# Kernel optimization log

Measured on AMD Instinct MI355X. Metric: run time of the kernel, lower is better.

Reference implementation:

```python
import jax, jax.numpy as jnp
import numpy as np

B, T, D = 64, 256, 1024
H, HS = 16, 64
FF = 4096
EPS = 1e-5


def _layernorm(x, g, b):
    mu = jnp.mean(x, axis=-1, keepdims=True)
    var = jnp.mean(jnp.square(x - mu), axis=-1, keepdims=True)
    return (x - mu) * jax.lax.rsqrt(var + EPS) * g + b


def setup_inputs() -> dict:
    key = jax.random.key(0)
    ks = jax.random.split(key, 12)
    s = 0.02
    return {
        "x": jax.random.normal(ks[0], (B, T, D), jnp.float32),
        "ln1_g": jnp.ones((D,), jnp.float32),
        "ln1_b": jnp.zeros((D,), jnp.float32),
        "Wq": jax.random.normal(ks[1], (H, D, HS), jnp.float32) * s,
        "Wk": jax.random.normal(ks[2], (H, D, HS), jnp.float32) * s,
        "Wv": jax.random.normal(ks[3], (H, D, HS), jnp.float32) * s,
        "Wproj": jax.random.normal(ks[4], (D, D), jnp.float32) * s,
        "bproj": jnp.zeros((D,), jnp.float32),
        "ln2_g": jnp.ones((D,), jnp.float32),
        "ln2_b": jnp.zeros((D,), jnp.float32),
        "W1": jax.random.normal(ks[5], (D, FF), jnp.float32) * s,
        "b1": jnp.zeros((FF,), jnp.float32),
        "W2": jax.random.normal(ks[6], (FF, D), jnp.float32) * s,
        "b2": jnp.zeros((D,), jnp.float32),
    }


def reference(x, ln1_g, ln1_b, Wq, Wk, Wv, Wproj, bproj, ln2_g, ln2_b, W1, b1, W2, b2):
    # x = ln1(x)
    h = _layernorm(x, ln1_g, ln1_b)
    # per-head Q/K/V projections, batched over heads
    q = jnp.einsum("btd,hde->bhte", h, Wq)
    k = jnp.einsum("btd,hde->bhte", h, Wk)
    v = jnp.einsum("btd,hde->bhte", h, Wv)
    # NOTE: source scales by C**-0.5 with C = input_size (D), not head_size
    scale = D ** -0.5
    scores = jnp.einsum("bhte,bhse->bhts", q, k) * scale
    causal = jnp.tril(jnp.ones((T, T), bool))
    scores = jnp.where(causal, scores, -jnp.inf)
    w = jax.nn.softmax(scores, axis=-1)  # dropout is identity in eval
    attn = jnp.einsum("bhts,bhse->bthe", w, v).reshape(x.shape[0], x.shape[1], H * HS)
    sa = attn @ Wproj + bproj
    # residual onto ln1 output (as written in source)
    y = h + sa
    h2 = _layernorm(y, ln2_g, ln2_b)
    ff = jax.nn.relu(h2 @ W1 + b1) @ W2 + b2
    return h2 + ff
```

## Files before the change

kernel.cpp:

```cpp
#include <hip/hip_runtime.h>

typedef __bf16 bf16x8 __attribute__((ext_vector_type(8)));
typedef float f32x4 __attribute__((ext_vector_type(4)));
typedef unsigned short ushort_t;

__device__ __forceinline__ ushort_t f2bf(float f) {
  unsigned int u = __float_as_uint(f);
  u += 0x7fffu + ((u >> 16) & 1u);
  return (ushort_t)(u >> 16);
}
__device__ __forceinline__ float bf2f(ushort_t u) {
  return __uint_as_float(((unsigned int)u) << 16);
}

__device__ __forceinline__ void gl_lds16(const ushort_t* g, const char* l) {
  __builtin_amdgcn_global_load_lds(
      (const __attribute__((address_space(1))) void*)g,
      (__attribute__((address_space(3))) void*)l, 16, 0, 0);
}

__global__ __launch_bounds__(256) void fill_k(float* __restrict__ p, long n, float v) {
  long i = (long)blockIdx.x * 256 + threadIdx.x;
  if (i < n) p[i] = v;
}

__global__ __launch_bounds__(256) void transpose_w(const float* __restrict__ in,
                                                   ushort_t* __restrict__ out,
                                                   int R, int C) {
  __shared__ float tile[32][33];
  const float* inb = in + (long)blockIdx.z * R * C;
  ushort_t* outb = out + (long)blockIdx.z * R * C;
  int r0 = blockIdx.x * 32, c0 = blockIdx.y * 32;
  int tx = threadIdx.x & 31, ty = threadIdx.x >> 5;
#pragma unroll
  for (int i = ty; i < 32; i += 8) tile[i][tx] = inb[(long)(r0 + i) * C + (c0 + tx)];
  __syncthreads();
#pragma unroll
  for (int i = ty; i < 32; i += 8) outb[(long)(c0 + i) * R + (r0 + tx)] = f2bf(tile[tx][i]);
}

template <bool BFIN>
__global__ __launch_bounds__(256) void ln_k(const void* __restrict__ xin,
                                            const float* __restrict__ g,
                                            const float* __restrict__ b,
                                            ushort_t* __restrict__ outU) {
  __shared__ float red[8];
  long row = blockIdx.x;
  int tid = threadIdx.x;
  float4 v;
  if constexpr (BFIN) {
    ushort4 u4 = ((const ushort4*)((const ushort_t*)xin + row * 1024))[tid];
    v = make_float4(bf2f(u4.x), bf2f(u4.y), bf2f(u4.z), bf2f(u4.w));
  } else {
    v = ((const float4*)((const float*)xin + row * 1024))[tid];
  }
  float s = v.x + v.y + v.z + v.w;
#pragma unroll
  for (int off = 32; off; off >>= 1) s += __shfl_xor(s, off);
  int w = tid >> 6;
  if ((tid & 63) == 0) red[w] = s;
  __syncthreads();
  float mean = (red[0] + red[1] + red[2] + red[3]) * (1.0f / 1024.0f);
  float dx = v.x - mean, dy = v.y - mean, dz = v.z - mean, dw = v.w - mean;
  float s2 = dx * dx + dy * dy + dz * dz + dw * dw;
#pragma unroll
  for (int off = 32; off; off >>= 1) s2 += __shfl_xor(s2, off);
  if ((tid & 63) == 0) red[4 + w] = s2;
  __syncthreads();
  float var = (red[4] + red[5] + red[6] + red[7]) * (1.0f / 1024.0f);
  float rstd = rsqrtf(var + 1e-5f);
  int c = tid * 4;
  ushort4 u;
  u.x = f2bf(dx * rstd * g[c + 0] + b[c + 0]);
  u.y = f2bf(dy * rstd * g[c + 1] + b[c + 1]);
  u.z = f2bf(dz * rstd * g[c + 2] + b[c + 2]);
  u.w = f2bf(dw * rstd * g[c + 3] + b[c + 3]);
  ((ushort4*)(outU + row * 1024))[tid] = u;
}

template <int EPI>
__global__ __launch_bounds__(512, 2) void gemm256(const ushort_t* __restrict__ A,
                                                  const ushort_t* __restrict__ Bt,
                                                  int M, int N, int K, int NBC,
                                                  const float* __restrict__ bias,
                                                  const ushort_t* __restrict__ resU,
                                                  float* __restrict__ outF,
                                                  ushort_t* __restrict__ outU,
                                                  ushort_t* __restrict__ outU2,
                                                  ushort_t* __restrict__ outU3) {
  __shared__ __align__(16) char lds[131072];
  const int tid = threadIdx.x;
  const int lane = tid & 63;
  const int w = tid >> 6;
  const int wr = w >> 2, wc = w & 3;
  const int g = lane >> 4, lr = lane & 15;
  const int cpx = gridDim.x >> 3;
  const int wg = (blockIdx.x & 7) * cpx + (blockIdx.x >> 3);
  const long m0 = (long)(wg / NBC) * 256;
  const long n0 = (long)(wg % NBC) * 256;
  const int srow = tid >> 3;
  const int sslot = (tid & 7) ^ (srow & 7);
  const ushort_t* sA = A + (m0 + srow) * (long)K + sslot * 8;
  const ushort_t* sB = Bt + (n0 + srow) * (long)K + sslot * 8;
  const int dA = tid * 16;
  const int dB = 32768 + tid * 16;
  const int abase = (wr * 128 + lr) * 128;
  const int bbase = 32768 + (wc * 64 + lr) * 128;
  const int s0 = g ^ (lr & 7);
  const int s1 = (4 + g) ^ (lr & 7);
  const int NT = K >> 6;

  f32x4 acc[8][4] = {};
  bf16x8 aR[4][2], bR[4][2];
  const char* rb;

#define STAGE_A(tile, half) do {                                          \
    const long _ko = (long)(tile) * 64;                                   \
    char* _d = lds + (((tile) & 1) << 16) + ((half) << 14) + dA;          \
    gl_lds16(sA + _ko + (long)(2 * (half)) * 64 * K, _d);                 \
    gl_lds16(sA + _ko + (long)(2 * (half) + 1) * 64 * K, _d + 8192);      \
  } while (0)
#define STAGE_B(tile, half) do {                                          \
    const long _ko = (long)(tile) * 64;                                   \
    char* _d = lds + (((tile) & 1) << 16) + ((half) << 14) + dB;          \
    gl_lds16(sB + _ko + (long)(2 * (half)) * 64 * K, _d);                 \
    gl_lds16(sB + _ko + (long)(2 * (half) + 1) * 64 * K, _d + 8192);      \
  } while (0)
#define RD_A(base_mf) do {                                                \
    _Pragma("unroll") for (int mf = 0; mf < 4; ++mf) {                    \
      aR[mf][0] = *(const bf16x8*)(rb + abase + ((base_mf) + mf) * 2048 + s0 * 16); \
      aR[mf][1] = *(const bf16x8*)(rb + abase + ((base_mf) + mf) * 2048 + s1 * 16); \
    } } while (0)
#define RD_B2(base_nf) do {                                               \
    _Pragma("unroll") for (int nf = 0; nf < 2; ++nf) {                    \
      bR[(base_nf) + nf][0] = *(const bf16x8*)(rb + bbase + ((base_nf) + nf) * 2048 + s0 * 16); \
      bR[(base_nf) + nf][1] = *(const bf16x8*)(rb + bbase + ((base_nf) + nf) * 2048 + s1 * 16); \
    } } while (0)
#define QUAD(MB, NB) do {                                                 \
    __builtin_amdgcn_s_setprio(1);                                        \
    _Pragma("unroll") for (int mf = 0; mf < 4; ++mf)                      \
      _Pragma("unroll") for (int nf = 0; nf < 2; ++nf) {                  \
        acc[(MB) + mf][(NB) + nf] = __builtin_amdgcn_mfma_f32_16x16x32_bf16(aR[mf][0], bR[(NB) + nf][0], acc[(MB) + mf][(NB) + nf], 0, 0, 0); \
        acc[(MB) + mf][(NB) + nf] = __builtin_amdgcn_mfma_f32_16x16x32_bf16(aR[mf][1], bR[(NB) + nf][1], acc[(MB) + mf][(NB) + nf], 0, 0, 0); \
      }                                                                   \
    __builtin_amdgcn_s_setprio(0); } while (0)
#define LGKM0 do {                                                        \
    asm volatile("s_waitcnt lgkmcnt(0)" ::: "memory");                    \
    __builtin_amdgcn_sched_barrier(0); } while (0)

  STAGE_B(0, 0); STAGE_B(0, 1); STAGE_A(0, 0); STAGE_A(0, 1);
  STAGE_B(1, 0); STAGE_B(1, 1); STAGE_A(1, 0);
  asm volatile("s_waitcnt vmcnt(6)" ::: "memory");
  __builtin_amdgcn_s_barrier();

  for (int t = 0; t < NT; t += 2) {
    const bool s2 = (t + 2 < NT), s3 = (t + 3 < NT);
    rb = lds;
    RD_A(0);
    RD_B2(0);
    STAGE_A(t + 1, 1);
    asm volatile("s_waitcnt lgkmcnt(8)" ::: "memory");
    __builtin_amdgcn_s_barrier();
    LGKM0;
    QUAD(0, 0);
    __builtin_amdgcn_s_barrier();
    RD_B2(2);
    __builtin_amdgcn_s_barrier();
    LGKM0;
    QUAD(0, 2);
    __builtin_amdgcn_s_barrier();
    if (s2) STAGE_B(t + 2, 0);
    RD_A(4);
    __builtin_amdgcn_s_barrier();
    LGKM0;
    QUAD(4, 2);
    __builtin_amdgcn_s_barrier();
    if (s2) { STAGE_B(t + 2, 1); STAGE_A(t + 2, 0); }
    __builtin_amdgcn_s_barrier();
    QUAD(4, 0);
    if (s2) asm volatile("s_waitcnt vmcnt(6)" ::: "memory");
    else    asm volatile("s_waitcnt vmcnt(0)" ::: "memory");
    __builtin_amdgcn_s_barrier();
    rb = lds + 65536;
    RD_A(0);
    RD_B2(0);
    if (s2) STAGE_A(t + 2, 1);
    asm volatile("s_waitcnt lgkmcnt(8)" ::: "memory");
    __builtin_amdgcn_s_barrier();
    LGKM0;
    QUAD(0, 0);
    __builtin_amdgcn_s_barrier();
    RD_B2(2);
    __builtin_amdgcn_s_barrier();
    LGKM0;
    QUAD(0, 2);
    __builtin_amdgcn_s_barrier();
    if (s3) STAGE_B(t + 3, 0);
    RD_A(4);
    __builtin_amdgcn_s_barrier();
    LGKM0;
    QUAD(4, 2);
    __builtin_amdgcn_s_barrier();
    if (s3) { STAGE_B(t + 3, 1); STAGE_A(t + 3, 0); }
    __builtin_amdgcn_s_barrier();
    QUAD(4, 0);
    if (s3) asm volatile("s_waitcnt vmcnt(6)" ::: "memory");
    else    asm volatile("s_waitcnt vmcnt(0)" ::: "memory");
    __builtin_amdgcn_s_barrier();
  }
#undef STAGE_A
#undef STAGE_B
#undef RD_A
#undef RD_B2
#undef QUAD
#undef LGKM0

  if constexpr (EPI == 3 || EPI == 5) {
    ushort_t* l16 = (ushort_t*)lds;
#pragma unroll
    for (int mf = 0; mf < 8; ++mf)
#pragma unroll
      for (int nf = 0; nf < 4; ++nf) {
        int col = wc * 64 + nf * 16 + lr;
        long gcol = n0 + col;
#pragma unroll
        for (int r = 0; r < 4; ++r) {
          int row = wr * 128 + mf * 16 + g * 4 + r;
          float v = acc[mf][nf][r] + bias[gcol];
          if constexpr (EPI == 3) v = fmaxf(v, 0.0f);
          else v += bf2f(resU[(m0 + row) * (long)N + gcol]);
          l16[row * 256 + (col ^ (g << 3))] = f2bf(v);
        }
      }
    __syncthreads();
#pragma unroll
    for (int k = 0; k < 16; ++k) {
      int c = tid + k * 512;
      int tt = c >> 5, off = c & 31;
      int pc = (off * 8) ^ ((((unsigned)tt >> 2) & 3) << 3);
      uint4 d = *(uint4*)&l16[tt * 256 + pc];
      *(uint4*)&outU[(m0 + tt) * (long)N + n0 + off * 8] = d;
    }
  } else if constexpr (EPI == 6) {
#pragma unroll
    for (int mf = 0; mf < 8; ++mf)
#pragma unroll
      for (int nf = 0; nf < 4; ++nf)
#pragma unroll
        for (int r = 0; r < 4; ++r) {
          long row = m0 + wr * 128 + mf * 16 + g * 4 + r;
          long col = n0 + wc * 64 + nf * 16 + lr;
          long i = row * (long)N + col;
          outF[i] = acc[mf][nf][r] + bias[col] + bf2f(resU[i]);
        }
  } else {
    const int p = (int)(n0 >> 10);
    const long bb2 = m0 >> 8;
    if (p < 2) {
      ushort_t* dst = (p == 0) ? outU : outU2;
      ushort_t* l16 = (ushort_t*)lds;
#pragma unroll
      for (int mf = 0; mf < 8; ++mf)
#pragma unroll
        for (int nf = 0; nf < 4; ++nf) {
          int col = wc * 64 + nf * 16 + lr;
#pragma unroll
          for (int r = 0; r < 4; ++r) {
            int row = wr * 128 + mf * 16 + g * 4 + r;
            l16[row * 256 + (col ^ (g << 3))] = f2bf(acc[mf][nf][r]);
          }
        }
      __syncthreads();
      const int hh0 = (int)((n0 & 1023) >> 6);
#pragma unroll
      for (int k = 0; k < 16; ++k) {
        int c = tid + k * 512;
        int hh_l = c >> 11, tt = (c >> 3) & 255, off = c & 7;
        int col = hh_l * 64 + off * 8;
        int pc = col ^ ((((unsigned)tt >> 2) & 3) << 3);
        uint4 d = *(uint4*)&l16[tt * 256 + pc];
        *(uint4*)&dst[(((bb2 * 16 + hh0 + hh_l) * 256 + tt) << 6) + off * 8] = d;
      }
    } else {
      unsigned int* l32 = (unsigned int*)lds;
#pragma unroll
      for (int mf = 0; mf < 8; ++mf)
#pragma unroll
        for (int nf = 0; nf < 4; ++nf)
#pragma unroll
          for (int r2 = 0; r2 < 2; ++r2) {
            int row = wr * 128 + mf * 16 + g * 4 + r2 * 2;
            int col = wc * 64 + nf * 16 + lr;
            unsigned int pk = (unsigned int)f2bf(acc[mf][nf][r2 * 2]) |
                              ((unsigned int)f2bf(acc[mf][nf][r2 * 2 + 1]) << 16);
            l32[col * 128 + ((row >> 1) ^ ((col & 7) << 2))] = pk;
          }
      __syncthreads();
      const long vcol0 = (n0 & 1023);
#pragma unroll
      for (int k = 0; k < 16; ++k) {
        int c = tid + k * 512;
        int e_l = c >> 5, k16 = c & 31;
        uint4 d = *(uint4*)&l32[e_l * 128 + ((k16 * 4) ^ ((e_l & 7) << 2))];
        long vc = vcol0 + e_l;
        long hh = vc >> 6, e = vc & 63;
        *(uint4*)&outU3[(((bb2 * 16 + hh) * 64 + e) << 8) + k16 * 8] = d;
      }
    }
  }
}

__global__ __launch_bounds__(64, 4) void attn_k(const ushort_t* __restrict__ q,
                                                const ushort_t* __restrict__ k,
                                                const ushort_t* __restrict__ vt,
                                                ushort_t* __restrict__ ao) {
  __shared__ __align__(16) ushort_t Ps[32][40];
  const int lane = threadIdx.x;
  const int g = lane >> 4, lr = lane & 15;
  const int blk = blockIdx.x;
  const int q8 = blk & 7;
  const int bh = blk >> 3;
  const int bb = bh >> 4, hh = bh & 15;
  const int q0 = q8 * 32;
  const ushort_t* qb = q + (long)bh * 256 * 64;
  const ushort_t* kb = k + (long)bh * 256 * 64;
  const ushort_t* vb = vt + (long)bh * 64 * 256;
  bf16x8 qf[2][2];
#pragma unroll
  for (int m = 0; m < 2; m++)
#pragma unroll
    for (int ks = 0; ks < 2; ks++)
      qf[m][ks] = *(const bf16x8*)(qb + (q0 + m * 16 + lr) * 64 + ks * 32 + g * 8);
  f32x4 o[2][4] = {};
  float mrow[2][4], lrow[2][4];
#pragma unroll
  for (int m = 0; m < 2; m++)
#pragma unroll
    for (int r = 0; r < 4; r++) { mrow[m][r] = -3.0e38f; lrow[m][r] = 0.0f; }
  const float sc2 = 0.04508422f;
  const int nkb = q8 + 1;
  for (int kbk = 0; kbk < nkb; kbk++) {
    f32x4 s[2][2] = {};
#pragma unroll
    for (int ks = 0; ks < 2; ks++) {
      bf16x8 kf[2];
#pragma unroll
      for (int n = 0; n < 2; n++)
        kf[n] = *(const bf16x8*)(kb + (kbk * 32 + n * 16 + lr) * 64 + ks * 32 + g * 8);
#pragma unroll
      for (int m = 0; m < 2; m++)
#pragma unroll
        for (int n = 0; n < 2; n++)
          s[m][n] = __builtin_amdgcn_mfma_f32_16x16x32_bf16(qf[m][ks], kf[n], s[m][n], 0, 0, 0);
    }
    bf16x8 vf[4];
#pragma unroll
    for (int n = 0; n < 4; n++)
      vf[n] = *(const bf16x8*)(vb + (n * 16 + lr) * 256 + kbk * 32 + g * 8);
    if (kbk == q8) {
#pragma unroll
      for (int m = 0; m < 2; m++)
#pragma unroll
        for (int n = 0; n < 2; n++)
#pragma unroll
          for (int r = 0; r < 4; r++) {
            int row = q0 + m * 16 + g * 4 + r;
            int col = kbk * 32 + n * 16 + lr;
            s[m][n][r] = (col <= row) ? s[m][n][r] * sc2 : -3.0e38f;
          }
    } else {
#pragma unroll
      for (int m = 0; m < 2; m++)
#pragma unroll
        for (int n = 0; n < 2; n++)
#pragma unroll
          for (int r = 0; r < 4; r++) s[m][n][r] *= sc2;
    }
    float mx[2][4];
    float growth = -3.0e38f;
#pragma unroll
    for (int m = 0; m < 2; m++)
#pragma unroll
      for (int r = 0; r < 4; r++) {
        float v = fmaxf(s[m][0][r], s[m][1][r]);
#pragma unroll
        for (int off = 8; off; off >>= 1) v = fmaxf(v, __shfl_xor(v, off));
        mx[m][r] = v;
        growth = fmaxf(growth, v - mrow[m][r]);
      }
    if (__any(growth > 8.0f)) {
#pragma unroll
      for (int m = 0; m < 2; m++)
#pragma unroll
        for (int r = 0; r < 4; r++) {
          float mn = fmaxf(mrow[m][r], mx[m][r]);
          float al = exp2f(mrow[m][r] - mn);
          mrow[m][r] = mn;
          lrow[m][r] *= al;
#pragma unroll
          for (int n = 0; n < 4; n++) o[m][n][r] *= al;
        }
    }
#pragma unroll
    for (int m = 0; m < 2; m++)
#pragma unroll
      for (int r = 0; r < 4; r++) {
        float rs = 0.0f;
#pragma unroll
        for (int n = 0; n < 2; n++) {
          float p = exp2f(s[m][n][r] - mrow[m][r]);
          s[m][n][r] = p;
          rs += p;
        }
#pragma unroll
        for (int off = 8; off; off >>= 1) rs += __shfl_xor(rs, off);
        lrow[m][r] += rs;
      }
#pragma unroll
    for (int m = 0; m < 2; m++)
#pragma unroll
      for (int n = 0; n < 2; n++)
#pragma unroll
        for (int r = 0; r < 4; r++)
          Ps[m * 16 + g * 4 + r][n * 16 + lr] = f2bf(s[m][n][r]);
#pragma unroll
    for (int m = 0; m < 2; m++) {
      bf16x8 pa = *(const bf16x8*)&Ps[m * 16 + lr][g * 8];
#pragma unroll
      for (int n = 0; n < 4; n++)
        o[m][n] = __builtin_amdgcn_mfma_f32_16x16x32_bf16(pa, vf[n], o[m][n], 0, 0, 0);
    }
  }
#pragma unroll
  for (int m = 0; m < 2; m++)
#pragma unroll
    for (int r = 0; r < 4; r++) {
      float inv = 1.0f / lrow[m][r];
      long t = q0 + m * 16 + g * 4 + r;
#pragma unroll
      for (int n = 0; n < 4; n++) {
        long e = n * 16 + lr;
        ao[((long)bb * 256 + t) * 1024 + hh * 64 + e] = f2bf(o[m][n][r] * inv);
      }
    }
}

extern "C" void kernel_launch(void* const* d_in, const int* in_sizes, int n_in,
                              void* d_out, int out_size, void* d_ws, size_t ws_size,
                              hipStream_t stream) {
  const float* x     = (const float*)d_in[0];
  const float* ln1g  = (const float*)d_in[1];
  const float* ln1b  = (const float*)d_in[2];
  const float* Wq    = (const float*)d_in[3];
  const float* Wk    = (const float*)d_in[4];
  const float* Wv    = (const float*)d_in[5];
  const float* Wproj = (const float*)d_in[6];
  const float* bproj = (const float*)d_in[7];
  const float* ln2g  = (const float*)d_in[8];
  const float* ln2b  = (const float*)d_in[9];
  const float* W1    = (const float*)d_in[10];
  const float* b1    = (const float*)d_in[11];
  const float* W2    = (const float*)d_in[12];
  const float* b2    = (const float*)d_in[13];

  const long NEED = 184L << 20;
  if (ws_size < (size_t)NEED) {
    fill_k<<<(out_size + 255) / 256, 256, 0, stream>>>((float*)d_out, out_size,
                                                       (float)(ws_size >> 20));
    return;
  }

  char* ws = (char*)d_ws;
  const long MB = 1 << 20;
  ushort_t* wqt = (ushort_t*)(ws + 0 * MB);
  ushort_t* wkt = (ushort_t*)(ws + 2 * MB);
  ushort_t* wvt = (ushort_t*)(ws + 4 * MB);
  ushort_t* wpt = (ushort_t*)(ws + 6 * MB);
  ushort_t* w1t = (ushort_t*)(ws + 8 * MB);
  ushort_t* w2t = (ushort_t*)(ws + 16 * MB);
  ushort_t* hb  = (ushort_t*)(ws + 24 * MB);
  ushort_t* qbf = (ushort_t*)(ws + 56 * MB);
  ushort_t* kbf = (ushort_t*)(ws + 88 * MB);
  ushort_t* vtb = (ushort_t*)(ws + 120 * MB);
  ushort_t* atb = (ushort_t*)(ws + 152 * MB);
  ushort_t* yb  = (ushort_t*)(ws + 56 * MB);
  ushort_t* ff1 = (ushort_t*)(ws + 56 * MB);

  transpose_w<<<dim3(32, 2, 16), 256, 0, stream>>>(Wq, wqt, 1024, 64);
  transpose_w<<<dim3(32, 2, 16), 256, 0, stream>>>(Wk, wkt, 1024, 64);
  transpose_w<<<dim3(32, 2, 16), 256, 0, stream>>>(Wv, wvt, 1024, 64);
  transpose_w<<<dim3(32, 32, 1), 256, 0, stream>>>(Wproj, wpt, 1024, 1024);
  transpose_w<<<dim3(32, 128, 1), 256, 0, stream>>>(W1, w1t, 1024, 4096);
  transpose_w<<<dim3(128, 32, 1), 256, 0, stream>>>(W2, w2t, 4096, 1024);

  ln_k<false><<<16384, 256, 0, stream>>>(x, ln1g, ln1b, hb);
  gemm256<4><<<768, 512, 0, stream>>>(hb, wqt, 16384, 3072, 1024, 12,
                                      nullptr, nullptr, nullptr, qbf, kbf, vtb);
  attn_k<<<8192, 64, 0, stream>>>(qbf, kbf, vtb, atb);
  gemm256<5><<<256, 512, 0, stream>>>(atb, wpt, 16384, 1024, 1024, 4,
                                      bproj, hb, nullptr, yb, nullptr, nullptr);
  ln_k<true><<<16384, 256, 0, stream>>>(yb, ln2g, ln2b, hb);
  gemm256<3><<<1024, 512, 0, stream>>>(hb, w1t, 16384, 4096, 1024, 16,
                                       b1, nullptr, nullptr, ff1, nullptr, nullptr);
  gemm256<6><<<256, 512, 0, stream>>>(ff1, w2t, 16384, 1024, 4096, 4,
                                      b2, hb, (float*)d_out, nullptr, nullptr, nullptr);
}
```

Measured before the change: 595.8 us.

## Simplify GEMM main loop to whole-tile staging and column-major tile order

The fine-grained 8-phase ping-pong schedule is replaced by a simpler loop. Each iteration reads the full A and B fragments from LDS at once, runs two halves of MFMAs, and issues the whole next-but-one tile's global-to-LDS loads between them. The workgroup-to-tile mapping also changes from row-major to column-major, so consecutive workgroups share B columns, which changes L2 reuse. The cost is more registers held for the A fragments and less interleaving of LDS reads with MFMAs, which could hurt occupancy or latency hiding.

Measured after the change: 604.0 us. Within noise of the previous version (+1.4%).

```diff
diff --git a/kernel.cpp b/kernel.cpp
--- a/kernel.cpp
+++ b/kernel.cpp
@@ -96,8 +96,9 @@
   const int g = lane >> 4, lr = lane & 15;
   const int cpx = gridDim.x >> 3;
   const int wg = (blockIdx.x & 7) * cpx + (blockIdx.x >> 3);
-  const long m0 = (long)(wg / NBC) * 256;
-  const long n0 = (long)(wg % NBC) * 256;
+  const int NBM = gridDim.x / NBC;
+  const long m0 = (long)(wg % NBM) * 256;
+  const long n0 = (long)(wg / NBM) * 256;
   const int srow = tid >> 3;
   const int sslot = (tid & 7) ^ (srow & 7);
   const ushort_t* sA = A + (m0 + srow) * (long)K + sslot * 8;
@@ -111,108 +112,65 @@
   const int NT = K >> 6;
 
   f32x4 acc[8][4] = {};
-  bf16x8 aR[4][2], bR[4][2];
+  bf16x8 aR[8][2], bR[4][2];
   const char* rb;
 
-#define STAGE_A(tile, half) do {                                          \
+#define STAGE_TILE(tile) do {                                             \
     const long _ko = (long)(tile) * 64;                                   \
-    char* _d = lds + (((tile) & 1) << 16) + ((half) << 14) + dA;          \
-    gl_lds16(sA + _ko + (long)(2 * (half)) * 64 * K, _d);                 \
-    gl_lds16(sA + _ko + (long)(2 * (half) + 1) * 64 * K, _d + 8192);      \
+    char* _d = lds + (((tile) & 1) << 16);                                \
+    gl_lds16(sA + _ko, _d + dA);                                          \
+    gl_lds16(sA + _ko + 64 * (long)K, _d + 8192 + dA);                    \
+    gl_lds16(sA + _ko + 128 * (long)K, _d + 16384 + dA);                  \
+    gl_lds16(sA + _ko + 192 * (long)K, _d + 24576 + dA);                  \
+    gl_lds16(sB + _ko, _d + dB);                                          \
+    gl_lds16(sB + _ko + 64 * (long)K, _d + 8192 + dB);                    \
+    gl_lds16(sB + _ko + 128 * (long)K, _d + 16384 + dB);                  \
+    gl_lds16(sB + _ko + 192 * (long)K, _d + 24576 + dB);                  \
   } while (0)
-#define STAGE_B(tile, half) do {                                          \
-    const long _ko = (long)(tile) * 64;                                   \
-    char* _d = lds + (((tile) & 1) << 16) + ((half) << 14) + dB;          \
-    gl_lds16(sB + _ko + (long)(2 * (half)) * 64 * K, _d);                 \
-    gl_lds16(sB + _ko + (long)(2 * (half) + 1) * 64 * K, _d + 8192);      \
-  } while (0)
-#define RD_A(base_mf) do {                                                \
-    _Pragma("unroll") for (int mf = 0; mf < 4; ++mf) {                    \
-      aR[mf][0] = *(const bf16x8*)(rb + abase + ((base_mf) + mf) * 2048 + s0 * 16); \
-      aR[mf][1] = *(const bf16x8*)(rb + abase + ((base_mf) + mf) * 2048 + s1 * 16); \
+#define RD_ALL do {                                                       \
+    _Pragma("unroll") for (int mf = 0; mf < 8; ++mf) {                    \
+      aR[mf][0] = *(const bf16x8*)(rb + abase + mf * 2048 + s0 * 16);     \
+      aR[mf][1] = *(const bf16x8*)(rb + abase + mf * 2048 + s1 * 16);     \
+    }                                                                     \
+    _Pragma("unroll") for (int nf = 0; nf < 4; ++nf) {                    \
+      bR[nf][0] = *(const bf16x8*)(rb + bbase + nf * 2048 + s0 * 16);     \
+      bR[nf][1] = *(const bf16x8*)(rb + bbase + nf * 2048 + s1 * 16);     \
     } } while (0)
-#define RD_B2(base_nf) do {                                               \
-    _Pragma("unroll") for (int nf = 0; nf < 2; ++nf) {                    \
-      bR[(base_nf) + nf][0] = *(const bf16x8*)(rb + bbase + ((base_nf) + nf) * 2048 + s0 * 16); \
-      bR[(base_nf) + nf][1] = *(const bf16x8*)(rb + bbase + ((base_nf) + nf) * 2048 + s1 * 16); \
-    } } while (0)
-#define QUAD(MB, NB) do {                                                 \
+#define QUAD32(NB) do {                                                   \
     __builtin_amdgcn_s_setprio(1);                                        \
-    _Pragma("unroll") for (int mf = 0; mf < 4; ++mf)                      \
+    _Pragma("unroll") for (int mf = 0; mf < 8; ++mf)                      \
       _Pragma("unroll") for (int nf = 0; nf < 2; ++nf) {                  \
-        acc[(MB) + mf][(NB) + nf] = __builtin_amdgcn_mfma_f32_16x16x32_bf16(aR[mf][0], bR[(NB) + nf][0], acc[(MB) + mf][(NB) + nf], 0, 0, 0); \
-        acc[(MB) + mf][(NB) + nf] = __builtin_amdgcn_mfma_f32_16x16x32_bf16(aR[mf][1], bR[(NB) + nf][1], acc[(MB) + mf][(NB) + nf], 0, 0, 0); \
+        acc[mf][(NB) + nf] = __builtin_amdgcn_mfma_f32_16x16x32_bf16(aR[mf][0], bR[(NB) + nf][0], acc[mf][(NB) + nf], 0, 0, 0); \
+        acc[mf][(NB) + nf] = __builtin_amdgcn_mfma_f32_16x16x32_bf16(aR[mf][1], bR[(NB) + nf][1], acc[mf][(NB) + nf], 0, 0, 0); \
       }                                                                   \
     __builtin_amdgcn_s_setprio(0); } while (0)
 #define LGKM0 do {                                                        \
     asm volatile("s_waitcnt lgkmcnt(0)" ::: "memory");                    \
     __builtin_amdgcn_sched_barrier(0); } while (0)
 
-  STAGE_B(0, 0); STAGE_B(0, 1); STAGE_A(0, 0); STAGE_A(0, 1);
-  STAGE_B(1, 0); STAGE_B(1, 1); STAGE_A(1, 0);
-  asm volatile("s_waitcnt vmcnt(6)" ::: "memory");
+  STAGE_TILE(0);
+  STAGE_TILE(1);
+  asm volatile("s_waitcnt vmcnt(8)" ::: "memory");
   __builtin_amdgcn_s_barrier();
 
-  for (int t = 0; t < NT; t += 2) {
-    const bool s2 = (t + 2 < NT), s3 = (t + 3 < NT);
-    rb = lds;
-    RD_A(0);
-    RD_B2(0);
-    STAGE_A(t + 1, 1);
-    asm volatile("s_waitcnt lgkmcnt(8)" ::: "memory");
+  int c = 0;
+  for (int t = 0; t < NT; ++t) {
+    rb = lds + c;
+    RD_ALL;
     __builtin_amdgcn_s_barrier();
     LGKM0;
-    QUAD(0, 0);
+    QUAD32(0);
     __builtin_amdgcn_s_barrier();
-    RD_B2(2);
+    if (t + 2 < NT) STAGE_TILE(t + 2);
+    QUAD32(2);
+    if (t + 2 < NT) asm volatile("s_waitcnt vmcnt(8)" ::: "memory");
+    else            asm volatile("s_waitcnt vmcnt(0)" ::: "memory");
     __builtin_amdgcn_s_barrier();
-    LGKM0;
-    QUAD(0, 2);
-    __builtin_amdgcn_s_barrier();
-    if (s2) STAGE_B(t + 2, 0);
-    RD_A(4);
-    __builtin_amdgcn_s_barrier();
-    LGKM0;
-    QUAD(4, 2);
-    __builtin_amdgcn_s_barrier();
-    if (s2) { STAGE_B(t + 2, 1); STAGE_A(t + 2, 0); }
-    __builtin_amdgcn_s_barrier();
-    QUAD(4, 0);
-    if (s2) asm volatile("s_waitcnt vmcnt(6)" ::: "memory");
-    else    asm volatile("s_waitcnt vmcnt(0)" ::: "memory");
-    __builtin_amdgcn_s_barrier();
-    rb = lds + 65536;
-    RD_A(0);
-    RD_B2(0);
-    if (s2) STAGE_A(t + 2, 1);
-    asm volatile("s_waitcnt lgkmcnt(8)" ::: "memory");
-    __builtin_amdgcn_s_barrier();
-    LGKM0;
-    QUAD(0, 0);
-    __builtin_amdgcn_s_barrier();
-    RD_B2(2);
-    __builtin_amdgcn_s_barrier();
-    LGKM0;
-    QUAD(0, 2);
-    __builtin_amdgcn_s_barrier();
-    if (s3) STAGE_B(t + 3, 0);
-    RD_A(4);
-    __builtin_amdgcn_s_barrier();
-    LGKM0;
-    QUAD(4, 2);
-    __builtin_amdgcn_s_barrier();
-    if (s3) { STAGE_B(t + 3, 1); STAGE_A(t + 3, 0); }
-    __builtin_amdgcn_s_barrier();
-    QUAD(4, 0);
-    if (s3) asm volatile("s_waitcnt vmcnt(6)" ::: "memory");
-    else    asm volatile("s_waitcnt vmcnt(0)" ::: "memory");
-    __builtin_amdgcn_s_barrier();
+    c ^= 65536;
   }
-#undef STAGE_A
-#undef STAGE_B
-#undef RD_A
-#undef RD_B2
-#undef QUAD
+#undef STAGE_TILE
+#undef RD_ALL
+#undef QUAD32
 #undef LGKM0
 
   if constexpr (EPI == 3 || EPI == 5) {
@@ -235,8 +193,8 @@
     __syncthreads();
 #pragma unroll
     for (int k = 0; k < 16; ++k) {
-      int c = tid + k * 512;
-      int tt = c >> 5, off = c & 31;
+      int c2 = tid + k * 512;
+      int tt = c2 >> 5, off = c2 & 31;
       int pc = (off * 8) ^ ((((unsigned)tt >> 2) & 3) << 3);
       uint4 d = *(uint4*)&l16[tt * 256 + pc];
       *(uint4*)&outU[(m0 + tt) * (long)N + n0 + off * 8] = d;
@@ -274,8 +232,8 @@
       const int hh0 = (int)((n0 & 1023) >> 6);
 #pragma unroll
       for (int k = 0; k < 16; ++k) {
-        int c = tid + k * 512;
-        int hh_l = c >> 11, tt = (c >> 3) & 255, off = c & 7;
+        int c2 = tid + k * 512;
+        int hh_l = c2 >> 11, tt = (c2 >> 3) & 255, off = c2 & 7;
         int col = hh_l * 64 + off * 8;
         int pc = col ^ ((((unsigned)tt >> 2) & 3) << 3);
         uint4 d = *(uint4*)&l16[tt * 256 + pc];
@@ -299,8 +257,8 @@
       const long vcol0 = (n0 & 1023);
 #pragma unroll
       for (int k = 0; k < 16; ++k) {
-        int c = tid + k * 512;
-        int e_l = c >> 5, k16 = c & 31;
+        int c2 = tid + k * 512;
+        int e_l = c2 >> 5, k16 = c2 & 31;
         uint4 d = *(uint4*)&l32[e_l * 128 + ((k16 * 4) ^ ((e_l & 7) << 2))];
         long vc = vcol0 + e_l;
         long hh = vc >> 6, e = vc & 63;
```

## Switch GEMM inner loop from 16x16x32 to 32x32x16 MFMA tiles

Applied to the files above, without the earlier changes.

Rewrites the 256x256 GEMM's per-wave compute to use 32x32x16 bf16 MFMA with 16-element accumulators instead of 16x16x32 tiles. LDS fragment reads, the swizzle offsets and every epilogue's row/column mapping are remapped to the 32x32 output layout. Each operand fragment is now reused across more output elements, so fewer LDS reads are needed per MFMA. Register pressure and swizzle bank-conflict behaviour change, and epilogue index math gets more complex.

Result: slower. 650.9 us (+9.2%).

```diff
diff --git a/kernel.cpp b/kernel.cpp
--- a/kernel.cpp
+++ b/kernel.cpp
@@ -2,6 +2,7 @@
 
 typedef __bf16 bf16x8 __attribute__((ext_vector_type(8)));
 typedef float f32x4 __attribute__((ext_vector_type(4)));
+typedef float f32x16 __attribute__((ext_vector_type(16)));
 typedef unsigned short ushort_t;
 
 __device__ __forceinline__ ushort_t f2bf(float f) {
@@ -93,6 +94,7 @@
   const int lane = tid & 63;
   const int w = tid >> 6;
   const int wr = w >> 2, wc = w & 3;
+  const int l31 = lane & 31, h = lane >> 5, l7 = lane & 7;
   const int g = lane >> 4, lr = lane & 15;
   const int cpx = gridDim.x >> 3;
   const int wg = (blockIdx.x & 7) * cpx + (blockIdx.x >> 3);
@@ -104,14 +106,15 @@
   const ushort_t* sB = Bt + (n0 + srow) * (long)K + sslot * 8;
   const int dA = tid * 16;
   const int dB = 32768 + tid * 16;
-  const int abase = (wr * 128 + lr) * 128;
-  const int bbase = 32768 + (wc * 64 + lr) * 128;
-  const int s0 = g ^ (lr & 7);
-  const int s1 = (4 + g) ^ (lr & 7);
+  const int arow = (wr * 128 + l31) * 128;
+  const int brow = 32768 + (wc * 64 + l31) * 128;
+  int axk[4];
+#pragma unroll
+  for (int kb = 0; kb < 4; ++kb) axk[kb] = ((kb * 2 + h) ^ l7) * 16;
   const int NT = K >> 6;
 
-  f32x4 acc[8][4] = {};
-  bf16x8 aR[4][2], bR[4][2];
+  f32x16 acc[4][2] = {};
+  bf16x8 aR[2][4], bR[2][4];
   const char* rb;
 
 #define STAGE_A(tile, half) do {                                          \
@@ -126,23 +129,21 @@
     gl_lds16(sB + _ko + (long)(2 * (half)) * 64 * K, _d);                 \
     gl_lds16(sB + _ko + (long)(2 * (half) + 1) * 64 * K, _d + 8192);      \
   } while (0)
-#define RD_A(base_mf) do {                                                \
-    _Pragma("unroll") for (int mf = 0; mf < 4; ++mf) {                    \
-      aR[mf][0] = *(const bf16x8*)(rb + abase + ((base_mf) + mf) * 2048 + s0 * 16); \
-      aR[mf][1] = *(const bf16x8*)(rb + abase + ((base_mf) + mf) * 2048 + s1 * 16); \
+#define RD_A(MB2) do {                                                    \
+    _Pragma("unroll") for (int kb = 0; kb < 4; ++kb) {                    \
+      aR[0][kb] = *(const bf16x8*)(rb + arow + (MB2) * 4096 + axk[kb]);   \
+      aR[1][kb] = *(const bf16x8*)(rb + arow + ((MB2) + 1) * 4096 + axk[kb]); \
     } } while (0)
-#define RD_B2(base_nf) do {                                               \
-    _Pragma("unroll") for (int nf = 0; nf < 2; ++nf) {                    \
-      bR[(base_nf) + nf][0] = *(const bf16x8*)(rb + bbase + ((base_nf) + nf) * 2048 + s0 * 16); \
-      bR[(base_nf) + nf][1] = *(const bf16x8*)(rb + bbase + ((base_nf) + nf) * 2048 + s1 * 16); \
-    } } while (0)
+#define RD_B(NB) do {                                                     \
+    _Pragma("unroll") for (int kb = 0; kb < 4; ++kb)                      \
+      bR[NB][kb] = *(const bf16x8*)(rb + brow + (NB) * 4096 + axk[kb]);   \
+  } while (0)
 #define QUAD(MB, NB) do {                                                 \
     __builtin_amdgcn_s_setprio(1);                                        \
-    _Pragma("unroll") for (int mf = 0; mf < 4; ++mf)                      \
-      _Pragma("unroll") for (int nf = 0; nf < 2; ++nf) {                  \
-        acc[(MB) + mf][(NB) + nf] = __builtin_amdgcn_mfma_f32_16x16x32_bf16(aR[mf][0], bR[(NB) + nf][0], acc[(MB) + mf][(NB) + nf], 0, 0, 0); \
-        acc[(MB) + mf][(NB) + nf] = __builtin_amdgcn_mfma_f32_16x16x32_bf16(aR[mf][1], bR[(NB) + nf][1], acc[(MB) + mf][(NB) + nf], 0, 0, 0); \
-      }                                                                   \
+    _Pragma("unroll") for (int kb = 0; kb < 4; ++kb) {                    \
+      acc[(MB)][NB] = __builtin_amdgcn_mfma_f32_32x32x16_bf16(aR[0][kb], bR[NB][kb], acc[(MB)][NB], 0, 0, 0); \
+      acc[(MB) + 1][NB] = __builtin_amdgcn_mfma_f32_32x32x16_bf16(aR[1][kb], bR[NB][kb], acc[(MB) + 1][NB], 0, 0, 0); \
+    }                                                                     \
     __builtin_amdgcn_s_setprio(0); } while (0)
 #define LGKM0 do {                                                        \
     asm volatile("s_waitcnt lgkmcnt(0)" ::: "memory");                    \
@@ -157,53 +158,53 @@
     const bool s2 = (t + 2 < NT), s3 = (t + 3 < NT);
     rb = lds;
     RD_A(0);
-    RD_B2(0);
+    RD_B(0);
     STAGE_A(t + 1, 1);
     asm volatile("s_waitcnt lgkmcnt(8)" ::: "memory");
     __builtin_amdgcn_s_barrier();
     LGKM0;
     QUAD(0, 0);
     __builtin_amdgcn_s_barrier();
-    RD_B2(2);
+    RD_B(1);
     __builtin_amdgcn_s_barrier();
     LGKM0;
-    QUAD(0, 2);
+    QUAD(0, 1);
     __builtin_amdgcn_s_barrier();
     if (s2) STAGE_B(t + 2, 0);
-    RD_A(4);
+    RD_A(2);
     __builtin_amdgcn_s_barrier();
     LGKM0;
-    QUAD(4, 2);
+    QUAD(2, 1);
     __builtin_amdgcn_s_barrier();
     if (s2) { STAGE_B(t + 2, 1); STAGE_A(t + 2, 0); }
     __builtin_amdgcn_s_barrier();
-    QUAD(4, 0);
+    QUAD(2, 0);
     if (s2) asm volatile("s_waitcnt vmcnt(6)" ::: "memory");
     else    asm volatile("s_waitcnt vmcnt(0)" ::: "memory");
     __builtin_amdgcn_s_barrier();
     rb = lds + 65536;
     RD_A(0);
-    RD_B2(0);
+    RD_B(0);
     if (s2) STAGE_A(t + 2, 1);
     asm volatile("s_waitcnt lgkmcnt(8)" ::: "memory");
     __builtin_amdgcn_s_barrier();
     LGKM0;
     QUAD(0, 0);
     __builtin_amdgcn_s_barrier();
-    RD_B2(2);
+    RD_B(1);
     __builtin_amdgcn_s_barrier();
     LGKM0;
-    QUAD(0, 2);
+    QUAD(0, 1);
     __builtin_amdgcn_s_barrier();
     if (s3) STAGE_B(t + 3, 0);
-    RD_A(4);
+    RD_A(2);
     __builtin_amdgcn_s_barrier();
     LGKM0;
-    QUAD(4, 2);
+    QUAD(2, 1);
     __builtin_amdgcn_s_barrier();
     if (s3) { STAGE_B(t + 3, 1); STAGE_A(t + 3, 0); }
     __builtin_amdgcn_s_barrier();
-    QUAD(4, 0);
+    QUAD(2, 0);
     if (s3) asm volatile("s_waitcnt vmcnt(6)" ::: "memory");
     else    asm volatile("s_waitcnt vmcnt(0)" ::: "memory");
     __builtin_amdgcn_s_barrier();
@@ -211,48 +212,49 @@
 #undef STAGE_A
 #undef STAGE_B
 #undef RD_A
-#undef RD_B2
+#undef RD_B
 #undef QUAD
 #undef LGKM0
 
   if constexpr (EPI == 3 || EPI == 5) {
     ushort_t* l16 = (ushort_t*)lds;
 #pragma unroll
-    for (int mf = 0; mf < 8; ++mf)
-#pragma unroll
-      for (int nf = 0; nf < 4; ++nf) {
-        int col = wc * 64 + nf * 16 + lr;
+    for (int mb = 0; mb < 4; ++mb)
+#pragma unroll
+      for (int nb = 0; nb < 2; ++nb) {
+        int col = wc * 64 + nb * 32 + l31;
         long gcol = n0 + col;
 #pragma unroll
-        for (int r = 0; r < 4; ++r) {
-          int row = wr * 128 + mf * 16 + g * 4 + r;
-          float v = acc[mf][nf][r] + bias[gcol];
+        for (int reg = 0; reg < 16; ++reg) {
+          int row = wr * 128 + mb * 32 + (reg & 3) + 8 * (reg >> 2) + 4 * h;
+          float v = acc[mb][nb][reg] + bias[gcol];
           if constexpr (EPI == 3) v = fmaxf(v, 0.0f);
           else v += bf2f(resU[(m0 + row) * (long)N + gcol]);
-          l16[row * 256 + (col ^ (g << 3))] = f2bf(v);
+          l16[row * 256 + (col ^ (((row >> 2) & 3) << 3))] = f2bf(v);
         }
       }
     __syncthreads();
 #pragma unroll
     for (int k = 0; k < 16; ++k) {
-      int c = tid + k * 512;
-      int tt = c >> 5, off = c & 31;
+      int c2 = tid + k * 512;
+      int tt = c2 >> 5, off = c2 & 31;
       int pc = (off * 8) ^ ((((unsigned)tt >> 2) & 3) << 3);
       uint4 d = *(uint4*)&l16[tt * 256 + pc];
       *(uint4*)&outU[(m0 + tt) * (long)N + n0 + off * 8] = d;
     }
   } else if constexpr (EPI == 6) {
 #pragma unroll
-    for (int mf = 0; mf < 8; ++mf)
-#pragma unroll
-      for (int nf = 0; nf < 4; ++nf)
-#pragma unroll
-        for (int r = 0; r < 4; ++r) {
-          long row = m0 + wr * 128 + mf * 16 + g * 4 + r;
-          long col = n0 + wc * 64 + nf * 16 + lr;
+    for (int mb = 0; mb < 4; ++mb)
+#pragma unroll
+      for (int nb = 0; nb < 2; ++nb) {
+        long col = n0 + wc * 64 + nb * 32 + l31;
+#pragma unroll
+        for (int reg = 0; reg < 16; ++reg) {
+          long row = m0 + wr * 128 + mb * 32 + (reg & 3) + 8 * (reg >> 2) + 4 * h;
           long i = row * (long)N + col;
-          outF[i] = acc[mf][nf][r] + bias[col] + bf2f(resU[i]);
+          outF[i] = acc[mb][nb][reg] + bias[col] + bf2f(resU[i]);
         }
+      }
   } else {
     const int p = (int)(n0 >> 10);
     const long bb2 = m0 >> 8;
@@ -260,22 +262,22 @@
       ushort_t* dst = (p == 0) ? outU : outU2;
       ushort_t* l16 = (ushort_t*)lds;
 #pragma unroll
-      for (int mf = 0; mf < 8; ++mf)
-#pragma unroll
-        for (int nf = 0; nf < 4; ++nf) {
-          int col = wc * 64 + nf * 16 + lr;
-#pragma unroll
-          for (int r = 0; r < 4; ++r) {
-            int row = wr * 128 + mf * 16 + g * 4 + r;
-            l16[row * 256 + (col ^ (g << 3))] = f2bf(acc[mf][nf][r]);
+      for (int mb = 0; mb < 4; ++mb)
+#pragma unroll
+        for (int nb = 0; nb < 2; ++nb) {
+          int col = wc * 64 + nb * 32 + l31;
+#pragma unroll
+          for (int reg = 0; reg < 16; ++reg) {
+            int row = wr * 128 + mb * 32 + (reg & 3) + 8 * (reg >> 2) + 4 * h;
+            l16[row * 256 + (col ^ (((row >> 2) & 3) << 3))] = f2bf(acc[mb][nb][reg]);
           }
         }
       __syncthreads();
       const int hh0 = (int)((n0 & 1023) >> 6);
 #pragma unroll
       for (int k = 0; k < 16; ++k) {
-        int c = tid + k * 512;
-        int hh_l = c >> 11, tt = (c >> 3) & 255, off = c & 7;
+        int c2 = tid + k * 512;
+        int hh_l = c2 >> 11, tt = (c2 >> 3) & 255, off = c2 & 7;
         int col = hh_l * 64 + off * 8;
         int pc = col ^ ((((unsigned)tt >> 2) & 3) << 3);
         uint4 d = *(uint4*)&l16[tt * 256 + pc];
@@ -284,23 +286,24 @@
     } else {
       unsigned int* l32 = (unsigned int*)lds;
 #pragma unroll
-      for (int mf = 0; mf < 8; ++mf)
-#pragma unroll
-        for (int nf = 0; nf < 4; ++nf)
-#pragma unroll
-          for (int r2 = 0; r2 < 2; ++r2) {
-            int row = wr * 128 + mf * 16 + g * 4 + r2 * 2;
-            int col = wc * 64 + nf * 16 + lr;
-            unsigned int pk = (unsigned int)f2bf(acc[mf][nf][r2 * 2]) |
-                              ((unsigned int)f2bf(acc[mf][nf][r2 * 2 + 1]) << 16);
+      for (int mb = 0; mb < 4; ++mb)
+#pragma unroll
+        for (int nb = 0; nb < 2; ++nb) {
+          int col = wc * 64 + nb * 32 + l31;
+#pragma unroll
+          for (int j = 0; j < 8; ++j) {
+            int row = wr * 128 + mb * 32 + 2 * (j & 1) + 8 * (j >> 1) + 4 * h;
+            unsigned int pk = (unsigned int)f2bf(acc[mb][nb][2 * j]) |
+                              ((unsigned int)f2bf(acc[mb][nb][2 * j + 1]) << 16);
             l32[col * 128 + ((row >> 1) ^ ((col & 7) << 2))] = pk;
           }
+        }
       __syncthreads();
       const long vcol0 = (n0 & 1023);
 #pragma unroll
       for (int k = 0; k < 16; ++k) {
-        int c = tid + k * 512;
-        int e_l = c >> 5, k16 = c & 31;
+        int c2 = tid + k * 512;
+        int e_l = c2 >> 5, k16 = c2 & 31;
         uint4 d = *(uint4*)&l32[e_l * 128 + ((k16 * 4) ^ ((e_l & 7) << 2))];
         long vc = vcol0 + e_l;
         long hh = vc >> 6, e = vc & 63;
```
